# Kernel tuning notes

Hardware: AMD Instinct MI355X
Metric: run time of the kernel (lower is better)

Reference implementation:

```python
import jax, jax.numpy as jnp
import numpy as np

NUM_LEVELS = 4
RADIUS = 4


def _sample1d(vol, x):
    """Linear interpolation along width with zeros padding (grid_sample bilinear,
    align_corners=True, on a height-1 image reduces to this).
    vol: [N, W], x: [N, S] absolute x-coordinates. Returns [N, S]."""
    W = vol.shape[1]
    x0 = jnp.floor(x)
    t = x - x0
    i0 = x0.astype(jnp.int32)
    i1 = i0 + 1

    def gather(i):
        v = jnp.take_along_axis(vol, jnp.clip(i, 0, W - 1), axis=1)
        return jnp.where((i >= 0) & (i < W), v, jnp.zeros_like(v))

    return gather(i0) * (1.0 - t) + gather(i1) * t


def setup_inputs() -> dict:
    key = jax.random.key(0)
    k1, k2, k3 = jax.random.split(key, 3)
    B, C, h, w = 4, 256, 96, 320
    fmap1 = jax.random.normal(k1, (B, C, h, w), dtype=jnp.float32)
    fmap2 = jax.random.normal(k2, (B, C, h, w), dtype=jnp.float32)
    # absolute x-coordinates of centroids, in [0, w-1]
    centroids_coords = jax.random.uniform(k3, (B, 1, h, w), dtype=jnp.float32) * (w - 1)
    return {"fmap1": fmap1, "fmap2": fmap2, "centroids_coords": centroids_coords}


def reference(fmap1, fmap2, centroids_coords):
    B, C, h, w = fmap1.shape
    # 1D correlation volume: dot product over channels, per row, all width pairs
    corr = jnp.einsum('bchw,bchv->bhwv', fmap1, fmap2)  # [B, h, w, w]
    corr = corr / jnp.sqrt(jnp.asarray(C, fmap1.dtype))
    vol = corr.reshape(B * h * w, w)  # [N, w], one 1D row-correlation per query pixel

    cent = centroids_coords.transpose(0, 2, 3, 1).reshape(B * h * w)  # [N]
    side = 2 * RADIUS + 1
    di = jnp.linspace(-RADIUS, RADIUS, side).astype(fmap1.dtype)  # [side]

    outs = []
    for lvl in range(NUM_LEVELS):
        x = cent[:, None] + di[None, :]  # [N, side] absolute coords at this level
        outs.append(_sample1d(vol, x).reshape(B, h, w, side))
        if lvl < NUM_LEVELS - 1:
            Wl = vol.shape[1]
            # avg_pool2d kernel (1,2) stride (1,2) along width
            vol = vol[:, : (Wl // 2) * 2].reshape(vol.shape[0], Wl // 2, 2).mean(axis=2)
            cent = cent / 2.0

    corr_features = jnp.concatenate(outs, axis=-1).transpose(0, 3, 1, 2)
    return corr_features  # [B, num_levels*(2r+1), h, w]
```

## Files before the change

kernel.cpp:

```cpp
#include <hip/hip_runtime.h>

#define W_ 320
#define H_ 96
#define B_ 4
#define C_ 256
#define CS (H_ * W_)
#define MT_ 160
#define PITCHD 17
#define PITCH 34
#define PITCHC 321
#define ABUF (MT_ * PITCH)
#define BBUF (W_ * PITCH)
#define TBUF (ABUF + BBUF)

typedef __attribute__((ext_vector_type(8))) short short8;
typedef __attribute__((ext_vector_type(4))) float f32x4;

static __device__ __forceinline__ unsigned f2bf(float f) {
  unsigned u = __builtin_bit_cast(unsigned, f);
  return (u + 0x7FFFu + ((u >> 16) & 1u)) >> 16;
}
static __device__ __forceinline__ unsigned pk(float a, float b) {
  unsigned r;
  asm("v_cvt_pk_bf16_f32 %0, %1, %2" : "=v"(r) : "v"(a), "v"(b));
  return r;
}
static __device__ __forceinline__ float bf2f(unsigned short h) {
  return __builtin_bit_cast(float, (unsigned)h << 16);
}
static __device__ __forceinline__ void bar_keepvm() {
  asm volatile("s_waitcnt lgkmcnt(0)\n\ts_barrier" ::: "memory");
}

union Frag { short8 s; uint4 u; };

__global__ __launch_bounds__(512, 2) void corr_row(
    const float* __restrict__ fmap1, const float* __restrict__ fmap2,
    const float* __restrict__ cents, float* __restrict__ out)
{
  __shared__ __align__(16) unsigned short smem[2 * TBUF];
  unsigned short* Csh = smem;

  const int tid  = threadIdx.x;
  const int lane = tid & 63;
  const int wv   = tid >> 6;
  const int mw   = wv >> 2;
  const int nw   = wv & 3;
  const int m    = lane & 15;
  const int quad = lane >> 4;

  const int i    = blockIdx.x;
  const int r    = ((i >> 4) << 3) | (i & 7);
  const int half = (i >> 3) & 1;
  const int b    = r / H_;
  const int hh   = r % H_;
  const int q0   = half * MT_;

  const float* Abase = fmap1 + ((size_t)b * C_ * H_ + hh) * W_ + q0;
  const float* Bbase = fmap2 + ((size_t)b * C_ * H_ + hh) * W_;

  const float* sp[4];
  int dsti[4];
  bool act[4];
#pragma unroll
  for (int p = 0; p < 4; ++p) {
    int it = tid + 512 * p;
    act[p] = (it < 1920);
    bool isA = (it < 640);
    int c2, k;
    if (isA) { c2 = it / 40; k = it % 40; }
    else     { int ib = it - 640; c2 = ib / 80; k = ib % 80; }
    if (!act[p]) { c2 = 0; k = 0; }
    sp[p]   = (isA ? Abase : Bbase) + (size_t)(2 * c2) * CS + 4 * k;
    dsti[p] = k * PITCHD + c2 + (isA ? 0 : ABUF / 2);
  }
  const int st1 = (tid < 128) ? 40 * PITCHD : 80 * PITCHD;

  f32x4 acc[5][5] = {};
  Frag fa[5];

  float4 g0[4][2], g1[4][2];

  auto issue = [&](int s, float4 (*g)[2]) {
#pragma unroll
    for (int p = 0; p < 4; ++p)
      if (act[p]) {
        const float* q = sp[p] + (size_t)(s * 32) * CS;
        g[p][0] = *(const float4*)q;
        g[p][1] = *(const float4*)(q + CS);
      }
  };
  auto stage = [&](int s, float4 (*g)[2]) {
    unsigned* buf = (unsigned*)(smem + (s & 1) * TBUF);
#pragma unroll
    for (int p = 0; p < 4; ++p)
      if (act[p]) {
        unsigned* d = buf + dsti[p];
        const int st = (p == 0) ? 40 * PITCHD : (p >= 2 ? 80 * PITCHD : st1);
        d[0]      = pk(g[p][0].x, g[p][1].x);
        d[st]     = pk(g[p][0].y, g[p][1].y);
        d[2 * st] = pk(g[p][0].z, g[p][1].z);
        d[3 * st] = pk(g[p][0].w, g[p][1].w);
      }
  };

  const int pbA = (m & 3) * 40 + mw * 20 + (m >> 2);
  const int pbB = (m & 3) * 80 + nw * 20 + (m >> 2);

  auto fragmfma = [&](int s) {
    const unsigned* buf = (const unsigned*)(smem + (s & 1) * TBUF);
#pragma unroll
    for (int mt = 0; mt < 5; ++mt) {
      const unsigned* pa = buf + (pbA + mt * 4) * PITCHD + quad * 4;
      fa[mt].u.x = pa[0]; fa[mt].u.y = pa[1]; fa[mt].u.z = pa[2]; fa[mt].u.w = pa[3];
    }
#pragma unroll
    for (int nt = 0; nt < 5; ++nt) {
      const unsigned* pb = buf + (ABUF / 2) + (pbB + nt * 4) * PITCHD + quad * 4;
      Frag fb;
      fb.u.x = pb[0]; fb.u.y = pb[1]; fb.u.z = pb[2]; fb.u.w = pb[3];
#pragma unroll
      for (int mt = 0; mt < 5; ++mt)
        acc[mt][nt] = __builtin_amdgcn_mfma_f32_16x16x32_bf16(
            fa[mt].s, fb.s, acc[mt][nt], 0, 0, 0);
    }
  };

  issue(0, g0);
  issue(1, g1);
#pragma unroll
  for (int hs = 0; hs < 8; ++hs) {
    if (hs & 1) {
      stage(hs, g1);
      bar_keepvm();
      if (hs < 6) issue(hs + 2, g1);
    } else {
      stage(hs, g0);
      bar_keepvm();
      if (hs < 6) issue(hs + 2, g0);
    }
    fragmfma(hs);
  }

#pragma unroll 1
  for (int chunk = 0; chunk < 2; ++chunk) {
    __syncthreads();
    if (mw == chunk) {
#pragma unroll
      for (int mt = 0; mt < 5; ++mt)
#pragma unroll
        for (int nt = 0; nt < 5; ++nt)
#pragma unroll
          for (int rr = 0; rr < 4; ++rr)
            Csh[(mt * 16 + quad * 4 + rr) * PITCHC + nw * 80 + nt * 16 + m] =
                (unsigned short)f2bf(acc[mt][nt][rr] * 0.0625f);
    }
    __syncthreads();
    if (tid < 320) {
      const int l = tid / 80;
      const int q = tid % 80;
      const int qg = q0 + chunk * 80 + q;
      const int Wl  = W_ >> l;
      const int mul = 1 << l;
      const float invm = 1.0f / (float)mul;
      const float cent = cents[(b * H_ + hh) * W_ + qg];
      const float cl = cent * invm;
      const unsigned short* crow = Csh + q * PITCHC;
      float* op = out + ((size_t)(b * 36 + l * 9) * H_ + hh) * W_ + qg;
#pragma unroll
      for (int j = 0; j < 9; ++j) {
        float x  = cl + (float)(j - 4);
        float x0 = floorf(x);
        float t  = x - x0;
        int i0 = (int)x0;
        float v0 = 0.0f, v1 = 0.0f;
        if (i0 >= 0 && i0 < Wl) {
          float s2 = 0.0f;
          for (int d = 0; d < mul; ++d) s2 += bf2f(crow[i0 * mul + d]);
          v0 = s2 * invm;
        }
        int i1 = i0 + 1;
        if (i1 >= 0 && i1 < Wl) {
          float s2 = 0.0f;
          for (int d = 0; d < mul; ++d) s2 += bf2f(crow[i1 * mul + d]);
          v1 = s2 * invm;
        }
        op[(size_t)j * H_ * W_] = v0 * (1.0f - t) + v1 * t;
      }
    }
  }
}

extern "C" void kernel_launch(void* const* d_in, const int* in_sizes, int n_in,
                              void* d_out, int out_size, void* d_ws, size_t ws_size,
                              hipStream_t stream) {
  const float* fmap1 = (const float*)d_in[0];
  const float* fmap2 = (const float*)d_in[1];
  const float* cents = (const float*)d_in[2];
  float* out = (float*)d_out;
  corr_row<<<dim3(768), 512, 0, stream>>>(fmap1, fmap2, cents, out);
}
```

Before: 336.8 us.

## Shrink query tile to 64 columns and raise occupancy to four blocks per CU

Each block now covers 64 query columns instead of 160, so the grid grows from 768 to 1920 blocks, with 5 tiles per row mapped across XCDs. Register accumulators drop from 5x5 to 2x5, and the shared staging layout uses padded row groups (GA/GB). Prefetch depth falls from two stages to one, which permits launch_bounds of 4 blocks per CU. The aim is better occupancy and less tail imbalance, at the cost of re-reading each fmap2 row 5 times instead of twice and hiding less load latency.

```diff
diff --git a/kernel.cpp b/kernel.cpp
--- a/kernel.cpp
+++ b/kernel.cpp
@@ -5,13 +5,14 @@
 #define B_ 4
 #define C_ 256
 #define CS (H_ * W_)
-#define MT_ 160
+#define MT_ 64
 #define PITCHD 17
-#define PITCH 34
+#define GA 24
+#define GB 88
+#define ADW (( (3*GA) + 16) * PITCHD)
+#define BDW (( (3*GB) + 80) * PITCHD)
+#define TBUFD (ADW + BDW)
 #define PITCHC 321
-#define ABUF (MT_ * PITCH)
-#define BBUF (W_ * PITCH)
-#define TBUF (ABUF + BBUF)
 
 typedef __attribute__((ext_vector_type(8))) short short8;
 typedef __attribute__((ext_vector_type(4))) float f32x4;
@@ -34,11 +35,11 @@
 
 union Frag { short8 s; uint4 u; };
 
-__global__ __launch_bounds__(512, 2) void corr_row(
+__global__ __launch_bounds__(512, 4) void corr_row(
     const float* __restrict__ fmap1, const float* __restrict__ fmap2,
     const float* __restrict__ cents, float* __restrict__ out)
 {
-  __shared__ __align__(16) unsigned short smem[2 * TBUF];
+  __shared__ __align__(16) unsigned short smem[2 * 2 * TBUFD];
   unsigned short* Csh = smem;
 
   const int tid  = threadIdx.x;
@@ -49,144 +50,128 @@
   const int m    = lane & 15;
   const int quad = lane >> 4;
 
-  const int i    = blockIdx.x;
-  const int r    = ((i >> 4) << 3) | (i & 7);
-  const int half = (i >> 3) & 1;
-  const int b    = r / H_;
-  const int hh   = r % H_;
-  const int q0   = half * MT_;
+  const int i   = blockIdx.x;
+  const int xcd = i & 7;
+  const int t   = i >> 3;
+  const int r   = (t / 5) * 8 + xcd;
+  const int mb  = t % 5;
+  const int b   = r / H_;
+  const int hh  = r % H_;
+  const int q0  = mb * MT_;
 
   const float* Abase = fmap1 + ((size_t)b * C_ * H_ + hh) * W_ + q0;
   const float* Bbase = fmap2 + ((size_t)b * C_ * H_ + hh) * W_;
 
-  const float* sp[4];
-  int dsti[4];
-  bool act[4];
+  const float* sp[3];
+  int dsti[3];
 #pragma unroll
-  for (int p = 0; p < 4; ++p) {
+  for (int p = 0; p < 3; ++p) {
     int it = tid + 512 * p;
-    act[p] = (it < 1920);
-    bool isA = (it < 640);
+    bool isA = (it < 256);
     int c2, k;
-    if (isA) { c2 = it / 40; k = it % 40; }
-    else     { int ib = it - 640; c2 = ib / 80; k = ib % 80; }
-    if (!act[p]) { c2 = 0; k = 0; }
+    if (isA) { c2 = it >> 4; k = it & 15; }
+    else     { int ib = it - 256; c2 = ib / 80; k = ib % 80; }
     sp[p]   = (isA ? Abase : Bbase) + (size_t)(2 * c2) * CS + 4 * k;
-    dsti[p] = k * PITCHD + c2 + (isA ? 0 : ABUF / 2);
+    dsti[p] = k * PITCHD + c2 + (isA ? 0 : ADW);
   }
-  const int st1 = (tid < 128) ? 40 * PITCHD : 80 * PITCHD;
+  const int jst0 = (tid < 256) ? GA * PITCHD : GB * PITCHD;
 
-  f32x4 acc[5][5] = {};
-  Frag fa[5];
+  f32x4 acc[2][5] = {};
+  Frag fa[2];
+  float4 g[3][2];
 
-  float4 g0[4][2], g1[4][2];
-
-  auto issue = [&](int s, float4 (*g)[2]) {
+  auto issue = [&](int s) {
 #pragma unroll
-    for (int p = 0; p < 4; ++p)
-      if (act[p]) {
-        const float* q = sp[p] + (size_t)(s * 32) * CS;
-        g[p][0] = *(const float4*)q;
-        g[p][1] = *(const float4*)(q + CS);
-      }
+    for (int p = 0; p < 3; ++p) {
+      const float* q = sp[p] + (size_t)(s * 32) * CS;
+      g[p][0] = *(const float4*)q;
+      g[p][1] = *(const float4*)(q + CS);
+    }
   };
-  auto stage = [&](int s, float4 (*g)[2]) {
-    unsigned* buf = (unsigned*)(smem + (s & 1) * TBUF);
+  auto stage = [&](int s) {
+    unsigned* buf = (unsigned*)smem + (s & 1) * TBUFD;
 #pragma unroll
-    for (int p = 0; p < 4; ++p)
-      if (act[p]) {
-        unsigned* d = buf + dsti[p];
-        const int st = (p == 0) ? 40 * PITCHD : (p >= 2 ? 80 * PITCHD : st1);
-        d[0]      = pk(g[p][0].x, g[p][1].x);
-        d[st]     = pk(g[p][0].y, g[p][1].y);
-        d[2 * st] = pk(g[p][0].z, g[p][1].z);
-        d[3 * st] = pk(g[p][0].w, g[p][1].w);
-      }
+    for (int p = 0; p < 3; ++p) {
+      unsigned* d = buf + dsti[p];
+      const int st = (p == 0) ? jst0 : GB * PITCHD;
+      d[0]      = pk(g[p][0].x, g[p][1].x);
+      d[st]     = pk(g[p][0].y, g[p][1].y);
+      d[2 * st] = pk(g[p][0].z, g[p][1].z);
+      d[3 * st] = pk(g[p][0].w, g[p][1].w);
+    }
   };
 
-  const int pbA = (m & 3) * 40 + mw * 20 + (m >> 2);
-  const int pbB = (m & 3) * 80 + nw * 20 + (m >> 2);
+  const int pbA = ((m & 3) * GA + mw * 8 + (m >> 2)) * PITCHD + quad * 4;
+  const int pbB = ADW + ((m & 3) * GB + nw * 20 + (m >> 2)) * PITCHD + quad * 4;
 
   auto fragmfma = [&](int s) {
-    const unsigned* buf = (const unsigned*)(smem + (s & 1) * TBUF);
+    const unsigned* buf = (const unsigned*)smem + (s & 1) * TBUFD;
 #pragma unroll
-    for (int mt = 0; mt < 5; ++mt) {
-      const unsigned* pa = buf + (pbA + mt * 4) * PITCHD + quad * 4;
+    for (int mt = 0; mt < 2; ++mt) {
+      const unsigned* pa = buf + pbA + mt * 4 * PITCHD;
       fa[mt].u.x = pa[0]; fa[mt].u.y = pa[1]; fa[mt].u.z = pa[2]; fa[mt].u.w = pa[3];
     }
 #pragma unroll
     for (int nt = 0; nt < 5; ++nt) {
-      const unsigned* pb = buf + (ABUF / 2) + (pbB + nt * 4) * PITCHD + quad * 4;
+      const unsigned* pb = buf + pbB + nt * 4 * PITCHD;
       Frag fb;
       fb.u.x = pb[0]; fb.u.y = pb[1]; fb.u.z = pb[2]; fb.u.w = pb[3];
 #pragma unroll
-      for (int mt = 0; mt < 5; ++mt)
+      for (int mt = 0; mt < 2; ++mt)
         acc[mt][nt] = __builtin_amdgcn_mfma_f32_16x16x32_bf16(
             fa[mt].s, fb.s, acc[mt][nt], 0, 0, 0);
     }
   };
 
-  issue(0, g0);
-  issue(1, g1);
+  issue(0);
 #pragma unroll
   for (int hs = 0; hs < 8; ++hs) {
-    if (hs & 1) {
-      stage(hs, g1);
-      bar_keepvm();
-      if (hs < 6) issue(hs + 2, g1);
-    } else {
-      stage(hs, g0);
-      bar_keepvm();
-      if (hs < 6) issue(hs + 2, g0);
-    }
+    stage(hs);
+    bar_keepvm();
+    if (hs < 7) issue(hs + 1);
     fragmfma(hs);
   }
 
-#pragma unroll 1
-  for (int chunk = 0; chunk < 2; ++chunk) {
-    __syncthreads();
-    if (mw == chunk) {
+  __syncthreads();
 #pragma unroll
-      for (int mt = 0; mt < 5; ++mt)
+  for (int mt = 0; mt < 2; ++mt)
 #pragma unroll
-        for (int nt = 0; nt < 5; ++nt)
+    for (int nt = 0; nt < 5; ++nt)
 #pragma unroll
-          for (int rr = 0; rr < 4; ++rr)
-            Csh[(mt * 16 + quad * 4 + rr) * PITCHC + nw * 80 + nt * 16 + m] =
-                (unsigned short)f2bf(acc[mt][nt][rr] * 0.0625f);
-    }
-    __syncthreads();
-    if (tid < 320) {
-      const int l = tid / 80;
-      const int q = tid % 80;
-      const int qg = q0 + chunk * 80 + q;
-      const int Wl  = W_ >> l;
-      const int mul = 1 << l;
-      const float invm = 1.0f / (float)mul;
-      const float cent = cents[(b * H_ + hh) * W_ + qg];
-      const float cl = cent * invm;
-      const unsigned short* crow = Csh + q * PITCHC;
-      float* op = out + ((size_t)(b * 36 + l * 9) * H_ + hh) * W_ + qg;
+      for (int rr = 0; rr < 4; ++rr)
+        Csh[(mw * 32 + mt * 16 + quad * 4 + rr) * PITCHC + nw * 80 + nt * 16 + m] =
+            (unsigned short)f2bf(acc[mt][nt][rr] * 0.0625f);
+  __syncthreads();
+  if (tid < 256) {
+    const int l = tid >> 6;
+    const int q = tid & 63;
+    const int qg = q0 + q;
+    const int Wl  = W_ >> l;
+    const int mul = 1 << l;
+    const float invm = 1.0f / (float)mul;
+    const float cent = cents[(b * H_ + hh) * W_ + qg];
+    const float cl = cent * invm;
+    const unsigned short* crow = Csh + q * PITCHC;
+    float* op = out + ((size_t)(b * 36 + l * 9) * H_ + hh) * W_ + qg;
 #pragma unroll
-      for (int j = 0; j < 9; ++j) {
-        float x  = cl + (float)(j - 4);
-        float x0 = floorf(x);
-        float t  = x - x0;
-        int i0 = (int)x0;
-        float v0 = 0.0f, v1 = 0.0f;
-        if (i0 >= 0 && i0 < Wl) {
-          float s2 = 0.0f;
-          for (int d = 0; d < mul; ++d) s2 += bf2f(crow[i0 * mul + d]);
-          v0 = s2 * invm;
-        }
-        int i1 = i0 + 1;
-        if (i1 >= 0 && i1 < Wl) {
-          float s2 = 0.0f;
-          for (int d = 0; d < mul; ++d) s2 += bf2f(crow[i1 * mul + d]);
-          v1 = s2 * invm;
-        }
-        op[(size_t)j * H_ * W_] = v0 * (1.0f - t) + v1 * t;
+    for (int j = 0; j < 9; ++j) {
+      float x  = cl + (float)(j - 4);
+      float x0 = floorf(x);
+      float t  = x - x0;
+      int i0 = (int)x0;
+      float v0 = 0.0f, v1 = 0.0f;
+      if (i0 >= 0 && i0 < Wl) {
+        float s2 = 0.0f;
+        for (int d = 0; d < mul; ++d) s2 += bf2f(crow[i0 * mul + d]);
+        v0 = s2 * invm;
       }
+      int i1 = i0 + 1;
+      if (i1 >= 0 && i1 < Wl) {
+        float s2 = 0.0f;
+        for (int d = 0; d < mul; ++d) s2 += bf2f(crow[i1 * mul + d]);
+        v1 = s2 * invm;
+      }
+      op[(size_t)j * H_ * W_] = v0 * (1.0f - t) + v1 * t;
     }
   }
 }
@@ -198,5 +183,5 @@
   const float* fmap2 = (const float*)d_in[1];
   const float* cents = (const float*)d_in[2];
   float* out = (float*)d_out;
-  corr_row<<<dim3(768), 512, 0, stream>>>(fmap1, fmap2, cents, out);
+  corr_row<<<dim3(1920), 512, 0, stream>>>(fmap1, fmap2, cents, out);
 }
```

After: 293.7 us. 1.15x faster.
